# Kernel tuning notes

Measured on AMD Instinct MI355X. Metric: run time of the kernel, lower is better.

The kernel has to match this reference:

```python
import jax, jax.numpy as jnp
import numpy as np

T = 32768       # sequence length (batch=1 in original forward)
DY = 63         # mark dim; input_size = DY + 1 = 64
D_IN = 64
H = 256         # hidden_size
OUT = 32        # out_size
NI = 1024       # number of inducing points


def _lstm_scan(x, w_ih, w_hh, b_ih, b_hh, reverse):
    """Single-direction LSTM over [T, D] input, batch=1. PyTorch gate order i,f,g,o."""
    xg = x @ w_ih.T + (b_ih + b_hh)  # [T, 4H], input projection precomputed

    def step(carry, xg_t):
        h, c = carry
        g = xg_t + h @ w_hh.T
        i, f, gg, o = jnp.split(g, 4)
        c = jax.nn.sigmoid(f) * c + jax.nn.sigmoid(i) * jnp.tanh(gg)
        h = jax.nn.sigmoid(o) * jnp.tanh(c)
        return (h, c), h

    init = (jnp.zeros((H,), x.dtype), jnp.zeros((H,), x.dtype))
    _, hs = jax.lax.scan(step, init, xg, reverse=reverse)
    return hs  # [T, H]


def _bilstm(x, layer_params):
    for (wf, uf, bif, bhf, wb, ub, bib, bhb) in layer_params:
        hf = _lstm_scan(x, wf, uf, bif, bhf, False)
        hb = _lstm_scan(x, wb, ub, bib, bhb, True)
        x = jnp.concatenate([hf, hb], axis=-1)  # [T, 2H]
    return x


def setup_inputs() -> dict:
    key = jax.random.key(0)
    ks = iter(jax.random.split(key, 24))
    s = 1.0 / np.sqrt(H)  # PyTorch LSTM uniform(-1/sqrt(H), 1/sqrt(H)) init
    def U(shape):
        return jax.random.uniform(next(ks), shape, jnp.float32, -s, s)
    inp = {
        "Y": jax.random.normal(next(ks), (T, DY), jnp.float32),
        "dT": jax.random.uniform(next(ks), (T,), jnp.float32),
        "induce_idx": jnp.sort(jax.random.randint(next(ks), (NI,), 0, T)),
        # layer 0: input D_IN; layer 1: input 2H (bidirectional)
        "w_ih_l0f": U((4 * H, D_IN)), "w_hh_l0f": U((4 * H, H)), "b_ih_l0f": U((4 * H,)), "b_hh_l0f": U((4 * H,)),
        "w_ih_l0b": U((4 * H, D_IN)), "w_hh_l0b": U((4 * H, H)), "b_ih_l0b": U((4 * H,)), "b_hh_l0b": U((4 * H,)),
        "w_ih_l1f": U((4 * H, 2 * H)), "w_hh_l1f": U((4 * H, H)), "b_ih_l1f": U((4 * H,)), "b_hh_l1f": U((4 * H,)),
        "w_ih_l1b": U((4 * H, 2 * H)), "w_hh_l1b": U((4 * H, H)), "b_ih_l1b": U((4 * H,)), "b_hh_l1b": U((4 * H,)),
        "fc_weight": jax.random.normal(next(ks), (2 * H, 2 * OUT), jnp.float32),
    }
    return inp


def reference(Y, dT, induce_idx,
              w_ih_l0f, w_hh_l0f, b_ih_l0f, b_hh_l0f,
              w_ih_l0b, w_hh_l0b, b_ih_l0b, b_hh_l0b,
              w_ih_l1f, w_hh_l1f, b_ih_l1f, b_hh_l1f,
              w_ih_l1b, w_hh_l1b, b_ih_l1b, b_hh_l1b,
              fc_weight):
    x = jnp.concatenate([Y, dT[:, None]], axis=1)  # [T, D_IN]
    layer_params = [
        (w_ih_l0f, w_hh_l0f, b_ih_l0f, b_hh_l0f, w_ih_l0b, w_hh_l0b, b_ih_l0b, b_hh_l0b),
        (w_ih_l1f, w_hh_l1f, b_ih_l1f, b_hh_l1f, w_ih_l1b, w_hh_l1b, b_ih_l1b, b_hh_l1b),
    ]
    h = _bilstm(x, layer_params)          # [T, 2H]
    out = h @ fc_weight                    # [T, 2*OUT]
    sel = out[induce_idx]                  # [NI, 2*OUT]
    return sel[:, :OUT], sel[:, OUT:]
```

## Files before the change

### kernel.cpp

```cpp
#include <hip/hip_runtime.h>

typedef unsigned int u32;
typedef unsigned short u16;
typedef _Float16 f16;
typedef _Float16 f16x2 __attribute__((ext_vector_type(2)));
typedef _Float16 f16x4 __attribute__((ext_vector_type(4)));

#define T_SEQ 32768

static const size_t OFF_DT   = 0;
static const size_t OFF_FLG  = 1024;
static const size_t OFF_MAP  = 4096;
static const size_t OFF_H1G  = 135168;
static const size_t OFF_BIAS = 1183744;
static const size_t OFF_FCW  = 1200128;
static const size_t OFF_WQ8  = 1331200;
static const size_t OFF_WIH0 = 3428352;
static const size_t OFF_WIH1 = 3690496;
static const size_t OFF_XQ   = 5787648;
static const size_t OFF_H0   = 9981952;
static const size_t OFF_XG   = 43536384;
static const size_t XG_DIR   = (size_t)T_SEQ * 1024 * 2;
static const size_t NEED_PAR = OFF_XG + 2 * XG_DIR;

__device__ __forceinline__ float bf2f(u16 u) {
  union { u32 i; float f; } v; v.i = ((u32)u) << 16; return v.f;
}
__device__ __forceinline__ u16 f2bf(float f) {
  union { float f; u32 i; } v; v.f = f;
  u32 u = v.i;
  return (u16)((u + 0x7fffu + ((u >> 16) & 1u)) >> 16);
}
__device__ __forceinline__ u32 packf2(float a, float b) {
  f16x2 p; p.x = (f16)a; p.y = (f16)b;
  return __builtin_bit_cast(u32, p);
}
__device__ __forceinline__ u32 bf2f2(u32 v) {
  union { u32 i; float f; } lo, hi;
  lo.i = v << 16; hi.i = v & 0xffff0000u;
  return packf2(lo.f, hi.f);
}
__device__ __forceinline__ float ldf(const void* p, size_t i, u32 isf) {
  return isf ? ((const float*)p)[i] : bf2f(((const u16*)p)[i]);
}
__device__ __forceinline__ float fdot2f(f16x2 a, f16x2 b, float c) {
#if __has_builtin(__builtin_amdgcn_fdot2)
  return __builtin_amdgcn_fdot2(a, b, c, false);
#else
  return c + (float)a.x * (float)b.x + (float)a.y * (float)b.y;
#endif
}
__device__ __forceinline__ float fdotu(u32 a, u32 b, float c) {
  return fdot2f(__builtin_bit_cast(f16x2, a), __builtin_bit_cast(f16x2, b), c);
}
__device__ __forceinline__ int sdot4(u32 a, u32 b, int c) {
#if __has_builtin(__builtin_amdgcn_sdot4)
  return __builtin_amdgcn_sdot4((int)a, (int)b, c, false);
#else
  int r = c;
#pragma unroll
  for (int j = 0; j < 4; ++j)
    r += (int)(signed char)(a >> (8 * j)) * (int)(signed char)(b >> (8 * j));
  return r;
#endif
}
__device__ __forceinline__ int dpp_xor1(int x) {
#if __has_builtin(__builtin_amdgcn_update_dpp)
  return __builtin_amdgcn_update_dpp(0, x, 0xB1, 0xF, 0xF, true);
#else
  return __shfl_xor(x, 1);
#endif
}
__device__ __forceinline__ int dpp_xor2(int x) {
#if __has_builtin(__builtin_amdgcn_update_dpp)
  return __builtin_amdgcn_update_dpp(0, x, 0x4E, 0xF, 0xF, true);
#else
  return __shfl_xor(x, 2);
#endif
}
template <int CTRL>
__device__ __forceinline__ float dpp_bcastf(float x) {
#if __has_builtin(__builtin_amdgcn_update_dpp)
  return __builtin_bit_cast(float,
      __builtin_amdgcn_update_dpp(0, __builtin_bit_cast(int, x), CTRL, 0xF, 0xF, true));
#else
  return __shfl(x, (threadIdx.x & ~3) + (CTRL & 3));
#endif
}
__device__ __forceinline__ float sigf(float x) {
  return __builtin_amdgcn_rcpf(1.0f + __builtin_amdgcn_exp2f(-1.4426950408889634f * x));
}
__device__ __forceinline__ float tanhf_fast(float x) {
  return 1.0f - 2.0f * __builtin_amdgcn_rcpf(1.0f + __builtin_amdgcn_exp2f(2.8853900817779268f * x));
}
__device__ __forceinline__ void wg_barrier_lds() {
  asm volatile("s_waitcnt lgkmcnt(0)" ::: "memory");
  __builtin_amdgcn_s_barrier();
  asm volatile("" ::: "memory");
}

__global__ void k_detect(const u16* __restrict__ probe, u32* __restrict__ dt) {
  __shared__ int cnt;
  if (threadIdx.x == 0) cnt = 0;
  __syncthreads();
  int bad = 0;
  for (int i = threadIdx.x; i < 8192; i += 256) {
    float v = bf2f(probe[i]);
    if (!(v * v <= 16.0f)) bad++;
  }
  atomicAdd(&cnt, bad);
  __syncthreads();
  if (threadIdx.x == 0) *dt = (cnt > 64) ? 1u : 0u;
}

__global__ void k_conv_pairs(const void* __restrict__ src, u32* __restrict__ dst,
                             int np, const u32* __restrict__ dtp) {
  u32 isf = *dtp;
  int i = blockIdx.x * 256 + threadIdx.x;
  if (i >= np) return;
  if (isf) {
    const float* s = (const float*)src;
    dst[i] = packf2(s[2 * i], s[2 * i + 1]);
  } else {
    dst[i] = bf2f2(((const u32*)src)[i]);
  }
}

__global__ void k_quant(const void* __restrict__ src, u32* __restrict__ dst,
                        const u32* __restrict__ dtp) {
  u32 isf = *dtp;
  int i = blockIdx.x * 256 + threadIdx.x;
  int row = i >> 6, c = i & 63;
  u32 out = 0;
#pragma unroll
  for (int j = 0; j < 4; ++j) {
    float w = ldf(src, (size_t)row * 256 + 4 * c + j, isf);
    int q = (int)rintf(w * 2048.0f);
    q = q > 127 ? 127 : (q < -127 ? -127 : q);
    out |= ((u32)(q & 0xff)) << (8 * j);
  }
  dst[i] = out;
}

__global__ void k_conv_misc(const void* bi0f, const void* bh0f, const void* bi0b, const void* bh0b,
                            const void* bi1f, const void* bh1f, const void* bi1b, const void* bh1b,
                            const void* fcb, float* __restrict__ bias, float* __restrict__ fcw,
                            u32* __restrict__ flags, int* __restrict__ map,
                            const u32* __restrict__ dtp) {
  u32 isf = *dtp;
  int i = blockIdx.x * 256 + threadIdx.x;
  if (i < 4096) {
    int ld = i >> 10, r = i & 1023;
    const void* bi; const void* bh;
    if (ld == 0)      { bi = bi0f; bh = bh0f; }
    else if (ld == 1) { bi = bi0b; bh = bh0b; }
    else if (ld == 2) { bi = bi1f; bh = bh1f; }
    else              { bi = bi1b; bh = bh1b; }
    bias[i] = ldf(bi, r, isf) + ldf(bh, r, isf);
  } else if (i < 36864) {
    fcw[i - 4096] = ldf(fcb, i - 4096, isf);
  } else if (i < 36992) {
    flags[i - 36864] = 0;
  } else if (i < 69760) {
    map[i - 36992] = -1;
  }
}

__global__ void k_conv_x(const void* __restrict__ Y, const void* __restrict__ dT,
                         u32* __restrict__ xq, const u32* __restrict__ dtp) {
  u32 isf = *dtp;
  int i = blockIdx.x * 256 + threadIdx.x;
  if (i >= T_SEQ * 32) return;
  int t = i >> 5, m = i & 31, k2 = 2 * m;
  float a = ldf(Y, (size_t)t * 63 + k2, isf);
  float b = (k2 + 1 < 63) ? ldf(Y, (size_t)t * 63 + k2 + 1, isf) : ldf(dT, t, isf);
  xq[i] = packf2(a, b);
}

__global__ void k_map_set(const int* __restrict__ idx, int* __restrict__ map) {
  int i = blockIdx.x * 256 + threadIdx.x;
  if (i < 1024) map[idx[i]] = i;
}

__global__ __launch_bounds__(256) void k_gemm(
    const u32* __restrict__ Aq, const u32* __restrict__ Wc,
    const float* __restrict__ bias, f16* __restrict__ xgT, int Kp, int rev) {
  int t0 = blockIdx.x << 6, r0 = blockIdx.y << 6;
  int tid = threadIdx.x, tx = tid & 15, ty = tid >> 4;
  __shared__ u32 As[64][33];
  __shared__ u32 Bs[64][33];
  float acc[4][4] = {};
  for (int kp0 = 0; kp0 < Kp; kp0 += 32) {
#pragma unroll
    for (int i = 0; i < 8; ++i) {
      int idx = tid + (i << 8);
      int row = idx >> 5, kp = idx & 31, kpg = kp0 + kp;
      As[row][kp] = Aq[(size_t)(t0 + row) * Kp + kpg];
      Bs[row][kp] = Wc[(size_t)(r0 + row) * Kp + kpg];
    }
    __syncthreads();
#pragma unroll 4
    for (int kk = 0; kk < 32; ++kk) {
      u32 av[4], bv[4];
#pragma unroll
      for (int i = 0; i < 4; ++i) av[i] = As[ty * 4 + i][kk];
#pragma unroll
      for (int i = 0; i < 4; ++i) bv[i] = Bs[tx * 4 + i][kk];
#pragma unroll
      for (int i = 0; i < 4; ++i)
#pragma unroll
        for (int j = 0; j < 4; ++j)
          acc[i][j] = fdotu(av[i], bv[j], acc[i][j]);
    }
    __syncthreads();
  }
  int tb = t0 + (ty << 2);
#pragma unroll
  for (int j = 0; j < 4; ++j) {
    int rr = r0 + tx * 4 + j;
    float b = bias[rr];
    f16 v0 = (f16)(acc[0][j] + b);
    f16 v1 = (f16)(acc[1][j] + b);
    f16 v2 = (f16)(acc[2][j] + b);
    f16 v3 = (f16)(acc[3][j] + b);
    size_t base = (size_t)rr * T_SEQ;
    f16x4 v;
    size_t pos;
    if (rev) { pos = base + (size_t)(T_SEQ - 4 - tb); v = (f16x4){v3, v2, v1, v0}; }
    else     { pos = base + (size_t)tb;               v = (f16x4){v0, v1, v2, v3}; }
    *(f16x4*)(xgT + pos) = v;
  }
}

__global__ __launch_bounds__(1024)
__attribute__((amdgpu_waves_per_eu(4, 4))) void k_recur2(
    const f16* __restrict__ xgT, const u32* __restrict__ wq,
    f16* __restrict__ h_full, f16* __restrict__ h1g,
    const int* __restrict__ map, int dir0) {
  const int dir = dir0 + blockIdx.x;
  const int tid = threadIdx.x;
  const int u = tid >> 2;
  const int qq = tid & 3;
  const u32* wqd = wq + ((size_t)dir << 16);

  __shared__ __align__(16) unsigned char hb8[2][256];

  u32 w0[16], w1[16], w2[16], w3[16];
  {
    const uint4* pw = (const uint4*)wqd;
    const int b0 = ((0 << 8) | u) * 16 + (qq << 2);
    const int b1 = ((1 << 8) | u) * 16 + (qq << 2);
    const int b2 = ((2 << 8) | u) * 16 + (qq << 2);
    const int b3 = ((3 << 8) | u) * 16 + (qq << 2);
#pragma unroll
    for (int i = 0; i < 4; ++i) {
      uint4 v0 = pw[b0 + i]; uint4 v1 = pw[b1 + i];
      uint4 v2 = pw[b2 + i]; uint4 v3 = pw[b3 + i];
      w0[4 * i] = v0.x; w0[4 * i + 1] = v0.y; w0[4 * i + 2] = v0.z; w0[4 * i + 3] = v0.w;
      w1[4 * i] = v1.x; w1[4 * i + 1] = v1.y; w1[4 * i + 2] = v1.z; w1[4 * i + 3] = v1.w;
      w2[4 * i] = v2.x; w2[4 * i + 1] = v2.y; w2[4 * i + 2] = v2.z; w2[4 * i + 3] = v2.w;
      w3[4 * i] = v3.x; w3[4 * i + 1] = v3.y; w3[4 * i + 2] = v3.z; w3[4 * i + 3] = v3.w;
    }
  }
#pragma unroll
  for (int i = 0; i < 16; ++i)
    asm volatile("" : "+v"(w0[i]), "+v"(w1[i]), "+v"(w2[i]), "+v"(w3[i]));

  if (tid < 128) ((u32*)hb8)[tid] = 0;

  const float ksc = 1.0f / (2048.0f * 127.0f);
  const float sk = (qq == 2) ? 2.8853900817779268f : -1.4426950408889634f;
  const float aa = (qq == 2) ? -2.0f : 1.0f;
  const float bb = (qq == 2) ? 1.0f : 0.0f;

  const f16* xg_d = xgT + (size_t)blockIdx.x * ((size_t)T_SEQ * 1024);
  const f16* xrow = xg_d + (size_t)((qq << 8) | u) * T_SEQ;

  const int tstep = dir ? -1 : 1;
  int t = dir ? (T_SEQ - 1) : 0;
  int mp = map ? map[t] : -1;
  float c_state = 0.f;

  f16* hout = h_full ? (h_full + (size_t)t * 512 + (dir << 8) + u) : nullptr;
  const ptrdiff_t hstride = (ptrdiff_t)tstep * 512;

  uint4 xcur = *(const uint4*)xrow;
  uint4 xnxt = xcur;

  __syncthreads();

  for (int ch = 0; ch < T_SEQ / 8; ++ch) {
    if (ch + 1 < T_SEQ / 8) xnxt = *(const uint4*)(xrow + (((size_t)ch + 1) << 3));
#pragma unroll
    for (int j = 0; j < 8; ++j) {
      u32 dw = (j >> 1) == 0 ? xcur.x : (j >> 1) == 1 ? xcur.y
             : (j >> 1) == 2 ? xcur.z : xcur.w;
      f16x2 pr = __builtin_bit_cast(f16x2, dw);
      float xb = (float)((j & 1) ? pr.y : pr.x);

      int ms = mp;
      if (map) {
        int tn = t + tstep;
        int idx2 = ((unsigned)tn < T_SEQ) ? tn : t;
        mp = map[idx2];
      }

      const uint4* hp = (const uint4*)(&hb8[j & 1][qq << 6]);
      uint4 hv0 = hp[0], hv1 = hp[1], hv2 = hp[2], hv3 = hp[3];
      int acc0 = 0, acc1 = 0, acc2 = 0, acc3 = 0;
#define DOT4Q(HV, K)                 \
      acc0 = sdot4(w0[K], HV, acc0); \
      acc1 = sdot4(w1[K], HV, acc1); \
      acc2 = sdot4(w2[K], HV, acc2); \
      acc3 = sdot4(w3[K], HV, acc3);
      DOT4Q(hv0.x, 0)  DOT4Q(hv0.y, 1)  DOT4Q(hv0.z, 2)  DOT4Q(hv0.w, 3)
      DOT4Q(hv1.x, 4)  DOT4Q(hv1.y, 5)  DOT4Q(hv1.z, 6)  DOT4Q(hv1.w, 7)
      DOT4Q(hv2.x, 8)  DOT4Q(hv2.y, 9)  DOT4Q(hv2.z, 10) DOT4Q(hv2.w, 11)
      DOT4Q(hv3.x, 12) DOT4Q(hv3.y, 13) DOT4Q(hv3.z, 14) DOT4Q(hv3.w, 15)
#undef DOT4Q
      int A = (qq & 1) ? acc1 : acc0;
      int B = (qq & 1) ? acc0 : acc1;
      A += dpp_xor1(B);
      int C = (qq & 1) ? acc3 : acc2;
      int D = (qq & 1) ? acc2 : acc3;
      C += dpp_xor1(D);
      int E = (qq & 2) ? C : A;
      int F = (qq & 2) ? A : C;
      E += dpp_xor2(F);

      float x = __builtin_fmaf((float)E, ksc, xb);
      float r = __builtin_amdgcn_rcpf(1.0f + __builtin_amdgcn_exp2f(sk * x));
      float g = __builtin_fmaf(aa, r, bb);
      float gi = dpp_bcastf<0x00>(g);
      float gf = dpp_bcastf<0x55>(g);
      float gg = dpp_bcastf<0xAA>(g);
      float go = dpp_bcastf<0xFF>(g);
      c_state = __builtin_fmaf(gf, c_state, gi * gg);
      float h = go * tanhf_fast(c_state);
      int q8 = (int)rintf(h * 127.0f);
      if (qq == 0) {
        hb8[(j & 1) ^ 1][u] = (unsigned char)(q8 & 0xff);
        if (hout) *hout = (f16)h;
        if (h1g && ms >= 0) h1g[(size_t)ms * 512 + (dir << 8) + u] = (f16)h;
      }
      wg_barrier_lds();
      t += tstep;
      hout += hstride;
    }
    xcur = xnxt;
  }
}

__global__ void k_fc(const f16* __restrict__ hbase, const int* __restrict__ mapn,
                     const int* __restrict__ idx, const float* __restrict__ fcw,
                     void* __restrict__ out, const u32* __restrict__ dtp) {
  u32 isf = *dtp;
  int n = blockIdx.x;
  int cc = threadIdx.x;
  int slot = mapn ? mapn[idx[n]] : idx[n];
  const f16* hp = hbase + (size_t)slot * 512;
  float acc = 0.f;
#pragma unroll 8
  for (int k = 0; k < 512; ++k) acc += (float)hp[k] * fcw[k * 64 + cc];
  int o = (cc < 32) ? (n * 32 + cc) : (32 * 1024 + n * 32 + (cc - 32));
  if (isf) ((float*)out)[o] = acc;
  else     ((u16*)out)[o]   = f2bf(acc);
}

extern "C" void kernel_launch(void* const* d_in, const int* in_sizes, int n_in,
                              void* d_out, int out_size, void* d_ws, size_t ws_size,
                              hipStream_t stream) {
  const void* Y        = d_in[0];
  const void* dT       = d_in[1];
  const int*  idx      = (const int*)d_in[2];
  const void* w_ih_l0f = d_in[3];
  const void* w_hh_l0f = d_in[4];
  const void* b_ih_l0f = d_in[5];
  const void* b_hh_l0f = d_in[6];
  const void* w_ih_l0b = d_in[7];
  const void* w_hh_l0b = d_in[8];
  const void* b_ih_l0b = d_in[9];
  const void* b_hh_l0b = d_in[10];
  const void* w_ih_l1f = d_in[11];
  const void* w_hh_l1f = d_in[12];
  const void* b_ih_l1f = d_in[13];
  const void* b_hh_l1f = d_in[14];
  const void* w_ih_l1b = d_in[15];
  const void* w_hh_l1b = d_in[16];
  const void* b_ih_l1b = d_in[17];
  const void* b_hh_l1b = d_in[18];
  const void* fcbf     = d_in[19];

  char* ws = (char*)d_ws;
  u32*  dt    = (u32*)(ws + OFF_DT);
  u32*  flags = (u32*)(ws + OFF_FLG);
  int*  map   = (int*)(ws + OFF_MAP);
  f16*  h1g   = (f16*)(ws + OFF_H1G);
  float* bias = (float*)(ws + OFF_BIAS);
  float* fcw  = (float*)(ws + OFF_FCW);
  u32*  wq8   = (u32*)(ws + OFF_WQ8);
  u32*  wih0  = (u32*)(ws + OFF_WIH0);
  u32*  wih1  = (u32*)(ws + OFF_WIH1);
  u32*  xq    = (u32*)(ws + OFF_XQ);
  f16*  h0    = (f16*)(ws + OFF_H0);
  f16*  xg    = (f16*)(ws + OFF_XG);
  f16*  xg1   = xg + XG_DIR / 2;

  const int par = (ws_size >= NEED_PAR) ? 1 : 0;

  k_detect<<<1, 256, 0, stream>>>((const u16*)w_hh_l0f, dt);
  k_quant<<<256, 256, 0, stream>>>(w_hh_l0f, wq8 + 0 * 65536, dt);
  k_quant<<<256, 256, 0, stream>>>(w_hh_l0b, wq8 + 1 * 65536, dt);
  k_quant<<<256, 256, 0, stream>>>(w_hh_l1f, wq8 + 2 * 65536, dt);
  k_quant<<<256, 256, 0, stream>>>(w_hh_l1b, wq8 + 3 * 65536, dt);
  k_conv_pairs<<<128, 256, 0, stream>>>(w_ih_l0f, wih0 + 0, 32768, dt);
  k_conv_pairs<<<128, 256, 0, stream>>>(w_ih_l0b, wih0 + 32768, 32768, dt);
  k_conv_pairs<<<1024, 256, 0, stream>>>(w_ih_l1f, wih1 + 0, 262144, dt);
  k_conv_pairs<<<1024, 256, 0, stream>>>(w_ih_l1b, wih1 + 262144, 262144, dt);
  k_conv_misc<<<273, 256, 0, stream>>>(b_ih_l0f, b_hh_l0f, b_ih_l0b, b_hh_l0b,
                                       b_ih_l1f, b_hh_l1f, b_ih_l1b, b_hh_l1b,
                                       fcbf, bias, fcw, flags, map, dt);
  k_conv_x<<<4096, 256, 0, stream>>>(Y, dT, xq, dt);
  k_map_set<<<4, 256, 0, stream>>>(idx, map);

  dim3 ggrid(T_SEQ / 64, 16);
  if (par) {
    k_gemm<<<ggrid, 256, 0, stream>>>(xq, wih0, bias, xg, 32, 0);
    k_gemm<<<ggrid, 256, 0, stream>>>(xq, wih0 + 32768, bias + 1024, xg1, 32, 1);
    k_recur2<<<2, 1024, 0, stream>>>(xg, wq8, h0, nullptr, nullptr, 0);
    k_gemm<<<ggrid, 256, 0, stream>>>((const u32*)h0, wih1, bias + 2048, xg, 256, 0);
    k_gemm<<<ggrid, 256, 0, stream>>>((const u32*)h0, wih1 + 262144, bias + 3072, xg1, 256, 1);
    k_recur2<<<2, 1024, 0, stream>>>(xg, wq8 + 2 * 65536, h0, nullptr, nullptr, 0);
    k_fc<<<1024, 64, 0, stream>>>(h0, nullptr, idx, fcw, d_out, dt);
  } else {
    k_gemm<<<ggrid, 256, 0, stream>>>(xq, wih0, bias, xg, 32, 0);
    k_recur2<<<1, 1024, 0, stream>>>(xg, wq8, h0, nullptr, nullptr, 0);
    k_gemm<<<ggrid, 256, 0, stream>>>(xq, wih0 + 32768, bias + 1024, xg, 32, 1);
    k_recur2<<<1, 1024, 0, stream>>>(xg, wq8, h0, nullptr, nullptr, 1);
    k_gemm<<<ggrid, 256, 0, stream>>>((const u32*)h0, wih1, bias + 2048, xg, 256, 0);
    k_recur2<<<1, 1024, 0, stream>>>(xg, wq8 + 2 * 65536, nullptr, h1g, map, 0);
    k_gemm<<<ggrid, 256, 0, stream>>>((const u32*)h0, wih1 + 262144, bias + 3072, xg, 256, 1);
    k_recur2<<<1, 1024, 0, stream>>>(xg, wq8 + 2 * 65536, nullptr, h1g, map, 1);
    k_fc<<<1024, 64, 0, stream>>>(h1g, map, idx, fcw, d_out, dt);
  }
}
```

Before: 60.14 ms.

## Redistribute recurrent matvec across 16-lane groups with single LDS vector load

Changes the thread-to-work mapping of the recurrent kernel: each 16-lane group now handles four hidden units, and every lane loads a single 16-byte slice of h from LDS instead of four. Each lane holds an XOR-swizzled set of weight slices and computes 16 partial dot products, which are reduced by a butterfly of DPP and ds_swizzle exchanges. The goal is to cut LDS read traffic and bank pressure on the serial per-step critical path, at the cost of a longer cross-lane reduction. The map and h1g checks also become a template parameter, removing runtime branches in the inner loop.

```diff
diff --git a/kernel.cpp b/kernel.cpp
--- a/kernel.cpp
+++ b/kernel.cpp
@@ -78,6 +78,20 @@
   return __shfl_xor(x, 2);
 #endif
 }
+__device__ __forceinline__ int dpp_ror8(int x) {
+#if __has_builtin(__builtin_amdgcn_update_dpp)
+  return __builtin_amdgcn_update_dpp(0, x, 0x128, 0xF, 0xF, true);
+#else
+  return __shfl_xor(x, 8);
+#endif
+}
+__device__ __forceinline__ int swz_xor4(int x) {
+#if __has_builtin(__builtin_amdgcn_ds_swizzle)
+  return __builtin_amdgcn_ds_swizzle(x, 0x101F);
+#else
+  return __shfl_xor(x, 4);
+#endif
+}
 template <int CTRL>
 __device__ __forceinline__ float dpp_bcastf(float x) {
 #if __has_builtin(__builtin_amdgcn_update_dpp)
@@ -86,9 +100,6 @@
 #else
   return __shfl(x, (threadIdx.x & ~3) + (CTRL & 3));
 #endif
-}
-__device__ __forceinline__ float sigf(float x) {
-  return __builtin_amdgcn_rcpf(1.0f + __builtin_amdgcn_exp2f(-1.4426950408889634f * x));
 }
 __device__ __forceinline__ float tanhf_fast(float x) {
   return 1.0f - 2.0f * __builtin_amdgcn_rcpf(1.0f + __builtin_amdgcn_exp2f(2.8853900817779268f * x));
@@ -232,6 +243,7 @@
   }
 }
 
+template <bool HASMAP>
 __global__ __launch_bounds__(1024)
 __attribute__((amdgpu_waves_per_eu(4, 4))) void k_recur2(
     const f16* __restrict__ xgT, const u32* __restrict__ wq,
@@ -239,46 +251,36 @@
     const int* __restrict__ map, int dir0) {
   const int dir = dir0 + blockIdx.x;
   const int tid = threadIdx.x;
-  const int u = tid >> 2;
-  const int qq = tid & 3;
+  const int g16 = tid >> 4;
+  const int s = tid & 15;
+  const int u = (g16 << 2) + (s >> 2);
   const u32* wqd = wq + ((size_t)dir << 16);
 
   __shared__ __align__(16) unsigned char hb8[2][256];
 
-  u32 w0[16], w1[16], w2[16], w3[16];
+  uint4 w[16];
   {
     const uint4* pw = (const uint4*)wqd;
-    const int b0 = ((0 << 8) | u) * 16 + (qq << 2);
-    const int b1 = ((1 << 8) | u) * 16 + (qq << 2);
-    const int b2 = ((2 << 8) | u) * 16 + (qq << 2);
-    const int b3 = ((3 << 8) | u) * 16 + (qq << 2);
-#pragma unroll
-    for (int i = 0; i < 4; ++i) {
-      uint4 v0 = pw[b0 + i]; uint4 v1 = pw[b1 + i];
-      uint4 v2 = pw[b2 + i]; uint4 v3 = pw[b3 + i];
-      w0[4 * i] = v0.x; w0[4 * i + 1] = v0.y; w0[4 * i + 2] = v0.z; w0[4 * i + 3] = v0.w;
-      w1[4 * i] = v1.x; w1[4 * i + 1] = v1.y; w1[4 * i + 2] = v1.z; w1[4 * i + 3] = v1.w;
-      w2[4 * i] = v2.x; w2[4 * i + 1] = v2.y; w2[4 * i + 2] = v2.z; w2[4 * i + 3] = v2.w;
-      w3[4 * i] = v3.x; w3[4 * i + 1] = v3.y; w3[4 * i + 2] = v3.z; w3[4 * i + 3] = v3.w;
+#pragma unroll
+    for (int t = 0; t < 16; ++t) {
+      int r = t ^ s;
+      w[t] = pw[(size_t)((((r & 3) << 8) + (g16 << 2) + (r >> 2)) * 16 + s)];
     }
   }
-#pragma unroll
-  for (int i = 0; i < 16; ++i)
-    asm volatile("" : "+v"(w0[i]), "+v"(w1[i]), "+v"(w2[i]), "+v"(w3[i]));
 
   if (tid < 128) ((u32*)hb8)[tid] = 0;
 
   const float ksc = 1.0f / (2048.0f * 127.0f);
-  const float sk = (qq == 2) ? 2.8853900817779268f : -1.4426950408889634f;
-  const float aa = (qq == 2) ? -2.0f : 1.0f;
-  const float bb = (qq == 2) ? 1.0f : 0.0f;
+  const float sk = ((s & 3) == 2) ? 2.8853900817779268f : -1.4426950408889634f;
+  const float aa = ((s & 3) == 2) ? -2.0f : 1.0f;
+  const float bb = ((s & 3) == 2) ? 1.0f : 0.0f;
 
   const f16* xg_d = xgT + (size_t)blockIdx.x * ((size_t)T_SEQ * 1024);
-  const f16* xrow = xg_d + (size_t)((qq << 8) | u) * T_SEQ;
+  const f16* xrow = xg_d + (size_t)(((s & 3) << 8) | u) * T_SEQ;
 
   const int tstep = dir ? -1 : 1;
   int t = dir ? (T_SEQ - 1) : 0;
-  int mp = map ? map[t] : -1;
+  int mp = HASMAP ? map[t] : -1;
   float c_state = 0.f;
 
   f16* hout = h_full ? (h_full + (size_t)t * 512 + (dir << 8) + u) : nullptr;
@@ -299,36 +301,42 @@
       float xb = (float)((j & 1) ? pr.y : pr.x);
 
       int ms = mp;
-      if (map) {
+      if (HASMAP) {
         int tn = t + tstep;
         int idx2 = ((unsigned)tn < T_SEQ) ? tn : t;
         mp = map[idx2];
       }
 
-      const uint4* hp = (const uint4*)(&hb8[j & 1][qq << 6]);
-      uint4 hv0 = hp[0], hv1 = hp[1], hv2 = hp[2], hv3 = hp[3];
-      int acc0 = 0, acc1 = 0, acc2 = 0, acc3 = 0;
-#define DOT4Q(HV, K)                 \
-      acc0 = sdot4(w0[K], HV, acc0); \
-      acc1 = sdot4(w1[K], HV, acc1); \
-      acc2 = sdot4(w2[K], HV, acc2); \
-      acc3 = sdot4(w3[K], HV, acc3);
-      DOT4Q(hv0.x, 0)  DOT4Q(hv0.y, 1)  DOT4Q(hv0.z, 2)  DOT4Q(hv0.w, 3)
-      DOT4Q(hv1.x, 4)  DOT4Q(hv1.y, 5)  DOT4Q(hv1.z, 6)  DOT4Q(hv1.w, 7)
-      DOT4Q(hv2.x, 8)  DOT4Q(hv2.y, 9)  DOT4Q(hv2.z, 10) DOT4Q(hv2.w, 11)
-      DOT4Q(hv3.x, 12) DOT4Q(hv3.y, 13) DOT4Q(hv3.z, 14) DOT4Q(hv3.w, 15)
-#undef DOT4Q
-      int A = (qq & 1) ? acc1 : acc0;
-      int B = (qq & 1) ? acc0 : acc1;
-      A += dpp_xor1(B);
-      int C = (qq & 1) ? acc3 : acc2;
-      int D = (qq & 1) ? acc2 : acc3;
-      C += dpp_xor1(D);
-      int E = (qq & 2) ? C : A;
-      int F = (qq & 2) ? A : C;
-      E += dpp_xor2(F);
-
-      float x = __builtin_fmaf((float)E, ksc, xb);
+      uint4 hv = ((const uint4*)hb8)[((j & 1) << 4) + s];
+
+      int a0, a1, a2, a3, a4, a5, a6, a7, a8, a9, a10, a11, a12, a13, a14, a15;
+#define DOTSLOT(A, T)                                             \
+      A = sdot4(w[T].w, hv.w,                                     \
+          sdot4(w[T].z, hv.z,                                     \
+          sdot4(w[T].y, hv.y,                                     \
+          sdot4(w[T].x, hv.x, 0))));
+      DOTSLOT(a0, 0)   DOTSLOT(a1, 1)   DOTSLOT(a2, 2)   DOTSLOT(a3, 3)
+      DOTSLOT(a4, 4)   DOTSLOT(a5, 5)   DOTSLOT(a6, 6)   DOTSLOT(a7, 7)
+      DOTSLOT(a8, 8)   DOTSLOT(a9, 9)   DOTSLOT(a10, 10) DOTSLOT(a11, 11)
+      DOTSLOT(a12, 12) DOTSLOT(a13, 13) DOTSLOT(a14, 14) DOTSLOT(a15, 15)
+#undef DOTSLOT
+      int b0 = a0 + dpp_xor1(a1);
+      int b1 = a2 + dpp_xor1(a3);
+      int b2 = a4 + dpp_xor1(a5);
+      int b3 = a6 + dpp_xor1(a7);
+      int b4 = a8 + dpp_xor1(a9);
+      int b5 = a10 + dpp_xor1(a11);
+      int b6 = a12 + dpp_xor1(a13);
+      int b7 = a14 + dpp_xor1(a15);
+      int c0 = b0 + dpp_xor2(b1);
+      int c1 = b2 + dpp_xor2(b3);
+      int c2 = b4 + dpp_xor2(b5);
+      int c3 = b6 + dpp_xor2(b7);
+      int d0 = c0 + swz_xor4(c1);
+      int d1 = c2 + swz_xor4(c3);
+      int e  = d0 + dpp_ror8(d1);
+
+      float x = __builtin_fmaf((float)e, ksc, xb);
       float r = __builtin_amdgcn_rcpf(1.0f + __builtin_amdgcn_exp2f(sk * x));
       float g = __builtin_fmaf(aa, r, bb);
       float gi = dpp_bcastf<0x00>(g);
@@ -338,10 +346,10 @@
       c_state = __builtin_fmaf(gf, c_state, gi * gg);
       float h = go * tanhf_fast(c_state);
       int q8 = (int)rintf(h * 127.0f);
-      if (qq == 0) {
+      if ((s & 3) == 0) {
         hb8[(j & 1) ^ 1][u] = (unsigned char)(q8 & 0xff);
-        if (hout) *hout = (f16)h;
-        if (h1g && ms >= 0) h1g[(size_t)ms * 512 + (dir << 8) + u] = (f16)h;
+        if (h_full) *hout = (f16)h;
+        if (HASMAP && ms >= 0) h1g[(size_t)ms * 512 + (dir << 8) + u] = (f16)h;
       }
       wg_barrier_lds();
       t += tstep;
@@ -427,20 +435,20 @@
   if (par) {
     k_gemm<<<ggrid, 256, 0, stream>>>(xq, wih0, bias, xg, 32, 0);
     k_gemm<<<ggrid, 256, 0, stream>>>(xq, wih0 + 32768, bias + 1024, xg1, 32, 1);
-    k_recur2<<<2, 1024, 0, stream>>>(xg, wq8, h0, nullptr, nullptr, 0);
+    k_recur2<false><<<2, 1024, 0, stream>>>(xg, wq8, h0, nullptr, nullptr, 0);
     k_gemm<<<ggrid, 256, 0, stream>>>((const u32*)h0, wih1, bias + 2048, xg, 256, 0);
     k_gemm<<<ggrid, 256, 0, stream>>>((const u32*)h0, wih1 + 262144, bias + 3072, xg1, 256, 1);
-    k_recur2<<<2, 1024, 0, stream>>>(xg, wq8 + 2 * 65536, h0, nullptr, nullptr, 0);
+    k_recur2<false><<<2, 1024, 0, stream>>>(xg, wq8 + 2 * 65536, h0, nullptr, nullptr, 0);
     k_fc<<<1024, 64, 0, stream>>>(h0, nullptr, idx, fcw, d_out, dt);
   } else {
     k_gemm<<<ggrid, 256, 0, stream>>>(xq, wih0, bias, xg, 32, 0);
-    k_recur2<<<1, 1024, 0, stream>>>(xg, wq8, h0, nullptr, nullptr, 0);
+    k_recur2<false><<<1, 1024, 0, stream>>>(xg, wq8, h0, nullptr, nullptr, 0);
     k_gemm<<<ggrid, 256, 0, stream>>>(xq, wih0 + 32768, bias + 1024, xg, 32, 1);
-    k_recur2<<<1, 1024, 0, stream>>>(xg, wq8, h0, nullptr, nullptr, 1);
+    k_recur2<false><<<1, 1024, 0, stream>>>(xg, wq8, h0, nullptr, nullptr, 1);
     k_gemm<<<ggrid, 256, 0, stream>>>((const u32*)h0, wih1, bias + 2048, xg, 256, 0);
-    k_recur2<<<1, 1024, 0, stream>>>(xg, wq8 + 2 * 65536, nullptr, h1g, map, 0);
+    k_recur2<true><<<1, 1024, 0, stream>>>(xg, wq8 + 2 * 65536, nullptr, h1g, map, 0);
     k_gemm<<<ggrid, 256, 0, stream>>>((const u32*)h0, wih1 + 262144, bias + 3072, xg, 256, 1);
-    k_recur2<<<1, 1024, 0, stream>>>(xg, wq8 + 2 * 65536, nullptr, h1g, map, 1);
+    k_recur2<true><<<1, 1024, 0, stream>>>(xg, wq8 + 2 * 65536, nullptr, h1g, map, 1);
     k_fc<<<1024, 64, 0, stream>>>(h1g, map, idx, fcw, d_out, dt);
   }
 }
```

Result: slower. 61.59 ms (+2.4%).
